# Optimization experiments

Measured on AMD Instinct MI355X. Metric: run time of the kernel, lower is better.

Reference implementation:

```python
import math
import jax, jax.numpy as jnp
import numpy as np

B, N, D, H, L = 8, 1024, 512, 8, 6
HD = D // H
FREQ = 256
K_LORENTZ = 1.0


def lorentz_projx(x, k=K_LORENTZ):
    # geoopt Lorentz.projx: x0 = sqrt(k + ||x_space||^2)
    space = x[..., 1:]
    x0 = jnp.sqrt(k + jnp.sum(space * space, axis=-1, keepdims=True))
    return jnp.concatenate([x0, space], axis=-1)


def layernorm(x, eps=1e-6):
    m = jnp.mean(x, axis=-1, keepdims=True)
    v = jnp.mean((x - m) ** 2, axis=-1, keepdims=True)
    return (x - m) / jnp.sqrt(v + eps)


def make_pe(n, d):
    pos = np.arange(n, dtype=np.float32)[:, None]
    div = np.exp(np.arange(0, d, 2, dtype=np.float32) * (-math.log(10000.0) / d))
    pe = np.zeros((n, d), dtype=np.float32)
    pe[:, 0::2] = np.sin(pos * div)
    pe[:, 1::2] = np.cos(pos * div)
    return jnp.asarray(pe)


def setup_inputs() -> dict:
    key = jax.random.key(0)
    ks = jax.random.split(key, 20)
    s = 0.02
    inp = {
        "t": jax.random.uniform(ks[0], (B,), jnp.float32) * 1000.0,
        "x": jax.random.normal(ks[1], (B, N, D), jnp.float32),
        "mask": jnp.ones((B, N), jnp.float32),
        "pe": make_pe(N, D),
        # timestep embedder MLP (weights stored [in,out])
        "tw1": jax.random.normal(ks[2], (FREQ, D), jnp.float32) * s,
        "tb1": jnp.zeros((D,), jnp.float32),
        "tw2": jax.random.normal(ks[3], (D, D), jnp.float32) * s,
        "tb2": jnp.zeros((D,), jnp.float32),
        # per-layer params stacked over L
        "Wq": jax.random.normal(ks[4], (L, D, D), jnp.float32) * s,
        "bq": jnp.zeros((L, D), jnp.float32),
        "Wk": jax.random.normal(ks[5], (L, D, D), jnp.float32) * s,
        "bk": jnp.zeros((L, D), jnp.float32),
        "Wv": jax.random.normal(ks[6], (L, D, D), jnp.float32) * s,
        "bv": jnp.zeros((L, D), jnp.float32),
        "W1": jax.random.normal(ks[7], (L, D, 4 * D), jnp.float32) * s,
        "b1": jnp.zeros((L, 4 * D), jnp.float32),
        "W2": jax.random.normal(ks[8], (L, 4 * D, D), jnp.float32) * s,
        "b2": jnp.zeros((L, D), jnp.float32),
        "Wada": jax.random.normal(ks[9], (L, D, 6 * D), jnp.float32) * s,
        "bada": jnp.zeros((L, 6 * D), jnp.float32),
    }
    return inp


def timestep_embedding(t, dim=FREQ, max_period=10000.0):
    half = dim // 2
    freqs = jnp.exp(-math.log(max_period) * jnp.arange(half, dtype=jnp.float32) / half)
    args = t[:, None] * freqs[None]
    return jnp.concatenate([jnp.cos(args), jnp.sin(args)], axis=-1)  # [B, dim]


def attention(h, mask, Wq, bq, Wk, bk, Wv, bv):
    # h: [B,N,D], mask: [B,N]
    q = (h @ Wq + bq).reshape(B, N, H, HD).transpose(0, 2, 1, 3)
    k = (h @ Wk + bk).reshape(B, N, H, HD).transpose(0, 2, 1, 3)
    v = (h @ Wv + bv).reshape(B, N, H, HD).transpose(0, 2, 1, 3)
    scores = jnp.einsum("bhqd,bhkd->bhqk", q, k) / math.sqrt(HD)
    # faithful quirk: valid positions get +1 added, invalid get -10000
    mm = jnp.einsum("bi,bj->bij", mask, mask)[:, None]  # [B,1,N,N]
    mm = jnp.where(mm == 0, -10000.0, mm)
    scores = scores + mm
    probs = jax.nn.softmax(scores, axis=-1)
    ctx = jnp.einsum("bhqk,bhkd->bhqd", probs, v)
    return ctx.transpose(0, 2, 1, 3).reshape(B, N, D)


def reference(t, x, mask, pe, tw1, tb1, tw2, tb2, Wq, bq, Wk, bk, Wv, bv,
              W1, b1, W2, b2, Wada, bada):
    # z = x + PositionalEncoding(x) = 2*x + pe
    z = x + (x + pe[None])
    # timestep embedder
    c = timestep_embedding(t) @ tw1 + tb1
    c = jax.nn.silu(c) @ tw2 + tb2  # [B, D]
    for i in range(L):
        ada = jax.nn.silu(c) @ Wada[i] + bada[i]  # [B, 6D]
        sh_msa, sc_msa, g_msa, sh_mlp, sc_mlp, g_mlp = jnp.split(ada, 6, axis=-1)
        h = layernorm(z) * (1.0 + sc_msa[:, None]) + sh_msa[:, None]
        z = z + g_msa[:, None] * attention(h, mask, Wq[i], bq[i], Wk[i], bk[i], Wv[i], bv[i])
        z = lorentz_projx(z)
        h = layernorm(z) * (1.0 + sc_mlp[:, None]) + sh_mlp[:, None]
        m = jax.nn.gelu(h @ W1[i] + b1[i], approximate=True) @ W2[i] + b2[i]
        z = z + g_mlp[:, None] * m
        z = lorentz_projx(z)
    z = lorentz_projx(z)
    return jnp.where(mask[:, :, None] != 0, z, 0.0)
```

## Files before the change

kernel.cpp:

```cpp
#include <hip/hip_runtime.h>
#include <hip/hip_bf16.h>
#include <math.h>

#define NTOK 1024
#define DMODEL 512
#define NHEAD 8
#define HDIM 64
#define BATCH 8
#define NLAYER 6
#define ROWS (BATCH*NTOK)
#define QKVSTR 1536
#define LOG2E 1.44269504f

typedef __attribute__((ext_vector_type(8))) short bf16x8;
typedef __attribute__((ext_vector_type(4))) float f32x4;
typedef unsigned short ushort_t;


__device__ __forceinline__ float silu_f(float x) { return x / (1.f + expf(-x)); }

__device__ __forceinline__ float gelu_tanh_f(float x) {
    float x3 = x * x * x;
    float y2 = 1.5957691216057308f * (x + 0.044715f * x3);
    float e = __builtin_amdgcn_exp2f(-y2 * LOG2E);
    return x / (1.f + e);
}

__device__ __forceinline__ unsigned short f2bf(float x) {
    __hip_bfloat16 b = __float2bfloat16(x);
    return *reinterpret_cast<unsigned short*>(&b);
}

__device__ __forceinline__ float bf2f(unsigned short u) {
    union { float f; unsigned v; } c;
    c.v = (unsigned)u << 16;
    return c.f;
}

template<int NW>
__device__ __forceinline__ float blk_sum(float v, volatile float* scratch) {
    #pragma unroll
    for (int o = 32; o > 0; o >>= 1) v += __shfl_down(v, o);
    if ((threadIdx.x & 63) == 0) scratch[threadIdx.x >> 6] = v;
    __syncthreads();
    float s = scratch[0];
    #pragma unroll
    for (int i = 1; i < NW; i++) s += scratch[i];
    __syncthreads();
    return s;
}


__global__ __launch_bounds__(256) void init_z_kernel(const float* __restrict__ x,
                                                     const float* __restrict__ pe,
                                                     float* __restrict__ z) {
    int i = blockIdx.x * 256 + threadIdx.x;
    const int C4 = DMODEL / 4;
    int row = i / C4;
    int col4 = i - row * C4;
    int n = row & (NTOK - 1);
    float4 xv = ((const float4*)x)[i];
    float4 pv = ((const float4*)pe)[n * C4 + col4];
    float4 o;
    o.x = 2.f * xv.x + pv.x;
    o.y = 2.f * xv.y + pv.y;
    o.z = 2.f * xv.z + pv.z;
    o.w = 2.f * xv.w + pv.w;
    ((float4*)z)[i] = o;
}

__global__ void temb_kernel(const float* __restrict__ t, float* __restrict__ temb) {
    int b = blockIdx.x;
    int j = threadIdx.x;
    float f = expf(-9.210340371976184f * (float)j / 128.f);
    float a = t[b] * f;
    temb[b * 256 + j] = cosf(a);
    temb[b * 256 + 128 + j] = sinf(a);
}

__global__ __launch_bounds__(256) void skinny_part(const float* __restrict__ A,
                                                   const float* __restrict__ W,
                                                   float* __restrict__ part,
                                                   int K, int N, int NL) {
    __shared__ float Als[8][128];
    const int l = blockIdx.z;
    const int n = blockIdx.x * 256 + threadIdx.x;
    const int kc = blockIdx.y;
    const int kbase = kc * 128;
    for (int i = threadIdx.x; i < 8 * 128; i += 256) {
        int b = i >> 7, k = i & 127;
        Als[b][k] = A[b * K + kbase + k];
    }
    __syncthreads();
    float acc[8] = {};
    const float* wp = W + (size_t)l * K * N + (size_t)kbase * N + n;
    for (int k = 0; k < 128; k += 4) {
        float w0 = wp[0];
        float w1 = wp[N];
        float w2 = wp[2 * N];
        float w3 = wp[3 * N];
        wp += 4 * (size_t)N;
        #pragma unroll
        for (int b = 0; b < 8; b++)
            acc[b] += Als[b][k] * w0 + Als[b][k + 1] * w1 + Als[b][k + 2] * w2 + Als[b][k + 3] * w3;
    }
    #pragma unroll
    for (int b = 0; b < 8; b++)
        part[((size_t)kc * 8 + b) * NL + (size_t)l * N + n] = acc[b];
}

template<int ACT>
__global__ __launch_bounds__(256) void skinny_reduce(const float* __restrict__ part,
                                                     const float* __restrict__ bias,
                                                     float* __restrict__ out,
                                                     int KC, int N, int NL) {
    int i = blockIdx.x * 256 + threadIdx.x;
    if (i >= 8 * NL) return;
    int b = i / NL, n = i - b * NL;
    float s = bias[n];
    for (int kc = 0; kc < KC; kc++) s += part[((size_t)kc * 8 + b) * NL + n];
    if (ACT == 1) s = silu_f(s);
    int l = n / N, nl = n - l * N;
    out[((size_t)l * 8 + b) * N + nl] = s;
}


__global__ __launch_bounds__(256) void transp_cvt3(const float* __restrict__ Wq,
                                                   const float* __restrict__ Wk,
                                                   const float* __restrict__ Wv,
                                                   ushort_t* __restrict__ dst) {
    __shared__ float tile[32][33];
    const float* src = blockIdx.z == 0 ? Wq : (blockIdx.z == 1 ? Wk : Wv);
    int k0 = blockIdx.y * 32, n0 = blockIdx.x * 32;
    int c = threadIdx.x & 31, r8 = threadIdx.x >> 5;
    #pragma unroll
    for (int i = 0; i < 4; i++) {
        int r = r8 + i * 8;
        tile[r][c] = src[(size_t)(k0 + r) * 512 + n0 + c];
    }
    __syncthreads();
    ushort_t* d = dst + (size_t)blockIdx.z * 512 * 512;
    #pragma unroll
    for (int i = 0; i < 4; i++) {
        int rr = r8 + i * 8;
        d[(size_t)(n0 + rr) * 512 + k0 + c] = f2bf(tile[c][rr]);
    }
}

__global__ __launch_bounds__(256) void transp_cvt(const float* __restrict__ src,
                                                  ushort_t* __restrict__ dst,
                                                  int K, int N) {
    __shared__ float tile[32][33];
    int k0 = blockIdx.y * 32, n0 = blockIdx.x * 32;
    int c = threadIdx.x & 31, r8 = threadIdx.x >> 5;
    #pragma unroll
    for (int i = 0; i < 4; i++) {
        int r = r8 + i * 8;
        tile[r][c] = src[(size_t)(k0 + r) * N + n0 + c];
    }
    __syncthreads();
    #pragma unroll
    for (int i = 0; i < 4; i++) {
        int rr = r8 + i * 8;
        dst[(size_t)(n0 + rr) * K + k0 + c] = f2bf(tile[c][rr]);
    }
}

__global__ void pack_bias(const float* __restrict__ bq, const float* __restrict__ bk,
                          const float* __restrict__ bv, float* __restrict__ bqkv) {
    int idx = blockIdx.x * 256 + threadIdx.x;
    if (idx >= NLAYER * QKVSTR) return;
    int l = idx / QKVSTR, n = idx - l * QKVSTR;
    float v = (n < 512) ? bq[l * 512 + n] : (n < 1024) ? bk[l * 512 + n - 512] : bv[l * 512 + n - 1024];
    bqkv[idx] = v;
}

template<int ACT, int OUTBF, int QPRESCALE>
__global__ __launch_bounds__(256) void mfma_gemm(const ushort_t* __restrict__ A,
                                                 const ushort_t* __restrict__ Bt,
                                                 const float* __restrict__ bias,
                                                 void* __restrict__ Cout,
                                                 int M, int N, int K) {
    __shared__ ushort_t Als[2][128 * 64];
    __shared__ ushort_t Bls[2][128 * 64];
    const int tid = threadIdx.x;
    const int lane = tid & 63, wv = tid >> 6;
    const int wm = (wv >> 1) * 64, wn = (wv & 1) * 64;
    const int lrow = lane & 15, lk = lane >> 4;
    const int m0 = blockIdx.x * 128, n0 = blockIdx.y * 128;
    const int srow = lane >> 3;
    const int qp = lane & 7;
    const int ql = qp ^ srow;

    f32x4 acc[4][4];
    #pragma unroll
    for (int i = 0; i < 4; i++)
        #pragma unroll
        for (int j = 0; j < 4; j++) {
            f32x4 zz = {0.f, 0.f, 0.f, 0.f};
            acc[i][j] = zz;
        }

    const int nK = K >> 6;

    auto STAGE = [&](int p, int ks) {
        const int k0 = ks << 6;
        #pragma unroll
        for (int it = 0; it < 4; it++) {
            int chunk = wv * 4 + it;
            int row = chunk * 8 + srow;
            const ushort_t* srcA = A + (size_t)(m0 + row) * K + k0 + ql * 8;
            const ushort_t* srcB = Bt + (size_t)(n0 + row) * K + k0 + ql * 8;
            __builtin_amdgcn_global_load_lds((const __attribute__((address_space(1))) void*)srcA,
                                             (__attribute__((address_space(3))) void*)(&Als[p][chunk * 512]),
                                             16, 0, 0);
            __builtin_amdgcn_global_load_lds((const __attribute__((address_space(1))) void*)srcB,
                                             (__attribute__((address_space(3))) void*)(&Bls[p][chunk * 512]),
                                             16, 0, 0);
        }
    };

    STAGE(0, 0);
    int cur = 0;
    for (int ks = 0; ks < nK; ks++) {
        if (ks + 1 < nK) {
            STAGE(cur ^ 1, ks + 1);
            asm volatile("s_waitcnt vmcnt(8)" ::: "memory");
        } else {
            asm volatile("s_waitcnt vmcnt(0)" ::: "memory");
        }
        __builtin_amdgcn_s_barrier();
        asm volatile("" ::: "memory");

        const ushort_t* Ab = &Als[cur][0];
        const ushort_t* Bb = &Bls[cur][0];
        #pragma unroll
        for (int kk = 0; kk < 2; kk++) {
            bf16x8 af[4], bfr[4];
            #pragma unroll
            for (int f = 0; f < 4; f++) {
                int ar = wm + f * 16 + lrow;
                af[f] = *(const bf16x8*)(Ab + ar * 64 + (((kk * 4 + lk) ^ (ar & 7)) << 3));
                int br = wn + f * 16 + lrow;
                bfr[f] = *(const bf16x8*)(Bb + br * 64 + (((kk * 4 + lk) ^ (br & 7)) << 3));
            }
            #pragma unroll
            for (int i = 0; i < 4; i++)
                #pragma unroll
                for (int j = 0; j < 4; j++)
                    acc[i][j] = __builtin_amdgcn_mfma_f32_16x16x32_bf16(af[i], bfr[j], acc[i][j], 0, 0, 0);
        }
        asm volatile("" ::: "memory");
        __builtin_amdgcn_s_barrier();
        cur ^= 1;
    }

    #pragma unroll
    for (int j = 0; j < 4; j++) {
        int col = n0 + wn + j * 16 + lrow;
        float bcol = bias[col];
        #pragma unroll
        for (int i = 0; i < 4; i++) {
            #pragma unroll
            for (int r = 0; r < 4; r++) {
                int row = m0 + wm + i * 16 + lk * 4 + r;
                float v = acc[i][j][r] + bcol;
                if (ACT == 1) v = gelu_tanh_f(v);
                if (QPRESCALE && col < 512) v *= 0.125f * LOG2E;
                if (OUTBF) ((ushort_t*)Cout)[(size_t)row * N + col] = f2bf(v);
                else       ((float*)Cout)[(size_t)row * N + col] = v;
            }
        }
    }
}


__global__ __launch_bounds__(128) void ln_mod_kernel(const float* __restrict__ z,
                                                     const float* __restrict__ ada,
                                                     ushort_t* __restrict__ out,
                                                     int sh_off, int sc_off) {
    __shared__ float red[2];
    int row = blockIdx.x;
    int b = row >> 10;
    int tid = threadIdx.x;
    float4 v = ((const float4*)(z + (size_t)row * DMODEL))[tid];
    float s = v.x + v.y + v.z + v.w;
    float mean = blk_sum<2>(s, red) * (1.f / DMODEL);
    float dx = v.x - mean, dy = v.y - mean, dz = v.z - mean, dw = v.w - mean;
    float ssq = dx * dx + dy * dy + dz * dz + dw * dw;
    float var = blk_sum<2>(ssq, red) * (1.f / DMODEL);
    float rstd = rsqrtf(var + 1e-6f);
    const float* ab = ada + b * (6 * DMODEL);
    float4 sc4 = ((const float4*)(ab + sc_off))[tid];
    float4 sh4 = ((const float4*)(ab + sh_off))[tid];
    unsigned short u0 = f2bf(dx * rstd * (1.f + sc4.x) + sh4.x);
    unsigned short u1 = f2bf(dy * rstd * (1.f + sc4.y) + sh4.y);
    unsigned short u2 = f2bf(dz * rstd * (1.f + sc4.z) + sh4.z);
    unsigned short u3 = f2bf(dw * rstd * (1.f + sc4.w) + sh4.w);
    uint2 pk;
    pk.x = (unsigned)u0 | ((unsigned)u1 << 16);
    pk.y = (unsigned)u2 | ((unsigned)u3 << 16);
    ((uint2*)(out + (size_t)row * DMODEL))[tid] = pk;
}

__global__ __launch_bounds__(128) void resid_ln_kernel(float* __restrict__ z,
                                                       const ushort_t* __restrict__ add,
                                                       const float* __restrict__ adaG, int g_off,
                                                       const float* __restrict__ adaLN, int sh_off, int sc_off,
                                                       ushort_t* __restrict__ out) {
    __shared__ float red[2];
    int row = blockIdx.x;
    int b = row >> 10;
    int tid = threadIdx.x;
    float4 v = ((float4*)(z + (size_t)row * DMODEL))[tid];
    uint2 a2 = ((const uint2*)(add + (size_t)row * DMODEL))[tid];
    float4 g4 = ((const float4*)(adaG + b * (6 * DMODEL) + g_off))[tid];
    v.x += g4.x * bf2f((unsigned short)(a2.x & 0xffff));
    v.y += g4.y * bf2f((unsigned short)(a2.x >> 16));
    v.z += g4.z * bf2f((unsigned short)(a2.y & 0xffff));
    v.w += g4.w * bf2f((unsigned short)(a2.y >> 16));
    float ssq = v.x * v.x + v.y * v.y + v.z * v.z + v.w * v.w;
    if (tid == 0) ssq -= v.x * v.x;
    float tot = blk_sum<2>(ssq, red);
    if (tid == 0) v.x = sqrtf(1.f + tot);
    ((float4*)(z + (size_t)row * DMODEL))[tid] = v;
    float s = v.x + v.y + v.z + v.w;
    float mean = blk_sum<2>(s, red) * (1.f / DMODEL);
    float dx = v.x - mean, dy = v.y - mean, dz = v.z - mean, dw = v.w - mean;
    float sq2 = dx * dx + dy * dy + dz * dz + dw * dw;
    float var = blk_sum<2>(sq2, red) * (1.f / DMODEL);
    float rstd = rsqrtf(var + 1e-6f);
    const float* ab = adaLN + b * (6 * DMODEL);
    float4 sc4 = ((const float4*)(ab + sc_off))[tid];
    float4 sh4 = ((const float4*)(ab + sh_off))[tid];
    unsigned short u0 = f2bf(dx * rstd * (1.f + sc4.x) + sh4.x);
    unsigned short u1 = f2bf(dy * rstd * (1.f + sc4.y) + sh4.y);
    unsigned short u2 = f2bf(dz * rstd * (1.f + sc4.z) + sh4.z);
    unsigned short u3 = f2bf(dw * rstd * (1.f + sc4.w) + sh4.w);
    uint2 pk;
    pk.x = (unsigned)u0 | ((unsigned)u1 << 16);
    pk.y = (unsigned)u2 | ((unsigned)u3 << 16);
    ((uint2*)(out + (size_t)row * DMODEL))[tid] = pk;
}

__global__ __launch_bounds__(128) void resid_final_kernel(const float* __restrict__ z,
                                                          const ushort_t* __restrict__ add,
                                                          const float* __restrict__ adaG, int g_off,
                                                          const float* __restrict__ mask,
                                                          float* __restrict__ out) {
    __shared__ float red[2];
    int row = blockIdx.x;
    int b = row >> 10;
    int tid = threadIdx.x;
    float4 v = ((const float4*)(z + (size_t)row * DMODEL))[tid];
    uint2 a2 = ((const uint2*)(add + (size_t)row * DMODEL))[tid];
    float4 g4 = ((const float4*)(adaG + b * (6 * DMODEL) + g_off))[tid];
    v.x += g4.x * bf2f((unsigned short)(a2.x & 0xffff));
    v.y += g4.y * bf2f((unsigned short)(a2.x >> 16));
    v.z += g4.z * bf2f((unsigned short)(a2.y & 0xffff));
    v.w += g4.w * bf2f((unsigned short)(a2.y >> 16));
    float ssq = v.x * v.x + v.y * v.y + v.z * v.z + v.w * v.w;
    if (tid == 0) ssq -= v.x * v.x;
    float tot = blk_sum<2>(ssq, red);
    if (tid == 0) v.x = sqrtf(1.f + tot);
    float m = mask[row];
    if (m == 0.f) { v.x = 0.f; v.y = 0.f; v.z = 0.f; v.w = 0.f; }
    ((float4*)(out + (size_t)row * DMODEL))[tid] = v;
}

__global__ __launch_bounds__(512) void flash_attn_mfma(const ushort_t* __restrict__ qkv,
                                                       const float* __restrict__ mask,
                                                       ushort_t* __restrict__ ctx) {
    __shared__ ushort_t Kls[64 * 64];
    __shared__ ushort_t Vt[64 * 64];
    __shared__ ushort_t Pls[8][16 * 64];
    __shared__ float Ms[64];

    const int tid = threadIdx.x;
    const int lane = tid & 63, w = tid >> 6;
    const int c = lane & 15, g = lane >> 4;
    const int bh = blockIdx.x;
    const int q0 = blockIdx.y * 128;
    const int b = bh >> 3, h = bh & 7;

    const ushort_t* qptr = qkv + (size_t)(b * NTOK + q0 + w * 16 + c) * QKVSTR + h * HDIM + g * 8;
    bf16x8 aq0 = *(const bf16x8*)(qptr);
    bf16x8 aq1 = *(const bf16x8*)(qptr + 32);

    const float mq = mask[b * NTOK + q0 + w * 16 + c];

    f32x4 o[4];
    #pragma unroll
    for (int j = 0; j < 4; j++) { f32x4 zz = {0.f,0.f,0.f,0.f}; o[j] = zz; }
    float m_run = -1e30f, l_run = 0.f;

    const int srow = lane >> 3, qp = lane & 7, ql = qp ^ srow;
    const int kp = tid & 31, dg = tid >> 5;

    char* Pw = (char*)&Pls[w][0];
    const int cswz = (c & 7) << 4;

    for (int kt = 0; kt < NTOK / 64; kt++) {
        const int k0 = kt * 64;
        __syncthreads();
        {
            int row = w * 8 + srow;
            const ushort_t* src = qkv + (size_t)(b * NTOK + k0 + row) * QKVSTR + 512 + h * HDIM + ql * 8;
            __builtin_amdgcn_global_load_lds((const __attribute__((address_space(1))) void*)src,
                                             (__attribute__((address_space(3))) void*)(Kls + w * 512),
                                             16, 0, 0);
        }
        {
            const ushort_t* v0 = qkv + (size_t)(b * NTOK + k0 + 2 * kp) * QKVSTR + 1024 + h * HDIM + dg * 4;
            uint2 r0 = *(const uint2*)v0;
            uint2 r1 = *(const uint2*)(v0 + QKVSTR);
            const ushort_t* e0 = (const ushort_t*)&r0;
            const ushort_t* e1 = (const ushort_t*)&r1;
            unsigned* VtU = (unsigned*)Vt;
            #pragma unroll
            for (int i = 0; i < 4; i++) {
                int d = dg * 4 + i;
                unsigned pk = (unsigned)e0[i] | ((unsigned)e1[i] << 16);
                VtU[d * 32 + (((kp >> 2) ^ (d & 7)) << 2) + (kp & 3)] = pk;
            }
        }
        if (tid < 64) Ms[tid] = mask[b * NTOK + k0 + tid];
        __syncthreads();

        f32x4 s[4];
        #pragma unroll
        for (int j = 0; j < 4; j++) { f32x4 zz = {0.f,0.f,0.f,0.f}; s[j] = zz; }
        __builtin_amdgcn_s_setprio(1);
        #pragma unroll
        for (int j = 0; j < 4; j++) {
            int row = j * 16 + c;
            bf16x8 ak0 = *(const bf16x8*)(Kls + row * 64 + ((g ^ (row & 7)) << 3));
            bf16x8 ak1 = *(const bf16x8*)(Kls + row * 64 + (((4 + g) ^ (row & 7)) << 3));
            s[j] = __builtin_amdgcn_mfma_f32_16x16x32_bf16(ak0, aq0, s[j], 0, 0, 0);
            s[j] = __builtin_amdgcn_mfma_f32_16x16x32_bf16(ak1, aq1, s[j], 0, 0, 0);
        }
        __builtin_amdgcn_s_setprio(0);

        float rm = -1e30f;
        #pragma unroll
        for (int j = 0; j < 4; j++) {
            float4 mk4 = *(const float4*)&Ms[j * 16 + 4 * g];
            const float* mkp = (const float*)&mk4;
            #pragma unroll
            for (int r = 0; r < 4; r++) {
                float mm = mq * mkp[r];
                s[j][r] += (mm == 0.f ? -14427.0f : mm * LOG2E);
                rm = fmaxf(rm, s[j][r]);
            }
        }
        rm = fmaxf(rm, __shfl_xor(rm, 16));
        rm = fmaxf(rm, __shfl_xor(rm, 32));

        if (!__all(rm - m_run <= 8.f)) {
            float mnew = fmaxf(m_run, rm);
            float scl = exp2f(m_run - mnew);
            m_run = mnew;
            float sclr[4];
            #pragma unroll
            for (int r = 0; r < 4; r++) sclr[r] = __shfl(scl, (g << 4) + 4 * g + r);
            #pragma unroll
            for (int j = 0; j < 4; j++)
                #pragma unroll
                for (int r = 0; r < 4; r++)
                    o[j][r] *= sclr[r];
            l_run *= scl;
        }

        float p[4][4];
        float rsum = 0.f;
        #pragma unroll
        for (int j = 0; j < 4; j++)
            #pragma unroll
            for (int r = 0; r < 4; r++) {
                p[j][r] = exp2f(s[j][r] - m_run);
                rsum += p[j][r];
            }
        rsum += __shfl_xor(rsum, 16);
        rsum += __shfl_xor(rsum, 32);
        l_run += rsum;

        #pragma unroll
        for (int j = 0; j < 4; j++) {
            uint2 pk2;
            pk2.x = (unsigned)f2bf(p[j][0]) | ((unsigned)f2bf(p[j][1]) << 16);
            pk2.y = (unsigned)f2bf(p[j][2]) | ((unsigned)f2bf(p[j][3]) << 16);
            *(uint2*)(Pw + c * 128 + ((j * 32 + g * 8) ^ cswz)) = pk2;
        }

        __builtin_amdgcn_s_setprio(1);
        #pragma unroll
        for (int kk = 0; kk < 2; kk++) {
            bf16x8 pa = *(const bf16x8*)(Pw + c * 128 + ((kk * 64 + g * 16) ^ cswz));
            #pragma unroll
            for (int j = 0; j < 4; j++) {
                int vr = j * 16 + c;
                bf16x8 bv = *(const bf16x8*)(Vt + vr * 64 + (((kk * 4 + g) ^ (vr & 7)) << 3));
                o[j] = __builtin_amdgcn_mfma_f32_16x16x32_bf16(pa, bv, o[j], 0, 0, 0);
            }
        }
        __builtin_amdgcn_s_setprio(0);
    }

    float invr[4];
    #pragma unroll
    for (int r = 0; r < 4; r++) invr[r] = 1.f / __shfl(l_run, (g << 4) + 4 * g + r);
    #pragma unroll
    for (int r = 0; r < 4; r++) {
        size_t row = (size_t)(b * NTOK + q0 + w * 16 + 4 * g + r) * DMODEL + h * HDIM;
        #pragma unroll
        for (int j = 0; j < 4; j++)
            ctx[row + j * 16 + c] = f2bf(o[j][r] * invr[r]);
    }
}


extern "C" void kernel_launch(void* const* d_in, const int* in_sizes, int n_in,
                              void* d_out, int out_size, void* d_ws, size_t ws_size,
                              hipStream_t stream) {
    const float* t    = (const float*)d_in[0];
    const float* x    = (const float*)d_in[1];
    const float* mask = (const float*)d_in[2];
    const float* pe   = (const float*)d_in[3];
    const float* tw1  = (const float*)d_in[4];
    const float* tb1  = (const float*)d_in[5];
    const float* tw2  = (const float*)d_in[6];
    const float* tb2  = (const float*)d_in[7];
    const float* Wq   = (const float*)d_in[8];
    const float* bq   = (const float*)d_in[9];
    const float* Wk   = (const float*)d_in[10];
    const float* bk   = (const float*)d_in[11];
    const float* Wv   = (const float*)d_in[12];
    const float* bv   = (const float*)d_in[13];
    const float* W1   = (const float*)d_in[14];
    const float* b1   = (const float*)d_in[15];
    const float* W2   = (const float*)d_in[16];
    const float* b2   = (const float*)d_in[17];
    const float* Wada = (const float*)d_in[18];
    const float* bada = (const float*)d_in[19];
    float* out = (float*)d_out;

    float* z      = (float*)d_ws;
    ushort_t* cxb = (ushort_t*)(z + (size_t)ROWS * DMODEL);
    ushort_t* qkv = cxb + (size_t)ROWS * DMODEL;
    ushort_t* mid = qkv;
    ushort_t* hb  = qkv + (size_t)ROWS * 2048;
    ushort_t* wqkv_t = hb + (size_t)ROWS * DMODEL;
    ushort_t* w1_t   = wqkv_t + 1536 * 512;
    ushort_t* w2_t   = w1_t + 2048 * 512;
    float* bqkv  = (float*)(w2_t + 512 * 2048);
    float* temb  = bqkv + NLAYER * QKVSTR;
    float* cmid  = temb + BATCH * 256;
    float* scs   = cmid + BATCH * DMODEL;
    float* part  = scs + BATCH * DMODEL;
    float* ada_all = part + 4 * 8 * (NLAYER * 3072);

    init_z_kernel<<<ROWS * DMODEL / 4 / 256, 256, 0, stream>>>(x, pe, z);
    temb_kernel<<<BATCH, 128, 0, stream>>>(t, temb);
    pack_bias<<<(NLAYER * QKVSTR + 255) / 256, 256, 0, stream>>>(bq, bk, bv, bqkv);

    skinny_part<<<dim3(2, 2, 1), 256, 0, stream>>>(temb, tw1, part, 256, 512, 512);
    skinny_reduce<1><<<16, 256, 0, stream>>>(part, tb1, cmid, 2, 512, 512);
    skinny_part<<<dim3(2, 4, 1), 256, 0, stream>>>(cmid, tw2, part, 512, 512, 512);
    skinny_reduce<1><<<16, 256, 0, stream>>>(part, tb2, scs, 4, 512, 512);
    skinny_part<<<dim3(12, 4, NLAYER), 256, 0, stream>>>(scs, Wada, part, 512, 3072, NLAYER * 3072);
    skinny_reduce<0><<<(8 * NLAYER * 3072 + 255) / 256, 256, 0, stream>>>(
        part, bada, ada_all, 4, 3072, NLAYER * 3072);

    dim3 gqkv(ROWS / 128, QKVSTR / 128);
    dim3 gmlp1(ROWS / 128, 2048 / 128);
    dim3 gmlp2(ROWS / 128, DMODEL / 128);
    dim3 ga(BATCH * NHEAD, NTOK / 128);

    ln_mod_kernel<<<ROWS, 128, 0, stream>>>(z, ada_all, hb, 0, 512);

    for (int i = 0; i < NLAYER; i++) {
        const float* ada = ada_all + (size_t)i * 8 * 3072;

        transp_cvt3<<<dim3(16, 16, 3), 256, 0, stream>>>(Wq + (size_t)i * 512 * 512,
                                                         Wk + (size_t)i * 512 * 512,
                                                         Wv + (size_t)i * 512 * 512, wqkv_t);
        transp_cvt<<<dim3(64, 16), 256, 0, stream>>>(W1 + (size_t)i * 512 * 2048, w1_t, 512, 2048);
        transp_cvt<<<dim3(16, 64), 256, 0, stream>>>(W2 + (size_t)i * 2048 * 512, w2_t, 2048, 512);

        mfma_gemm<0, 1, 1><<<gqkv, 256, 0, stream>>>(hb, wqkv_t, bqkv + i * QKVSTR, qkv,
                                                     ROWS, QKVSTR, DMODEL);

        flash_attn_mfma<<<ga, 512, 0, stream>>>(qkv, mask, cxb);

        resid_ln_kernel<<<ROWS, 128, 0, stream>>>(z, cxb, ada, 2 * DMODEL,
                                                  ada, 3 * DMODEL, 4 * DMODEL, hb);

        mfma_gemm<1, 1, 0><<<gmlp1, 256, 0, stream>>>(hb, w1_t, b1 + (size_t)i * 4 * DMODEL, mid,
                                                      ROWS, 4 * DMODEL, DMODEL);
        mfma_gemm<0, 1, 0><<<gmlp2, 256, 0, stream>>>(mid, w2_t, b2 + (size_t)i * DMODEL, cxb,
                                                      ROWS, DMODEL, 4 * DMODEL);

        if (i < NLAYER - 1) {
            const float* adan = ada_all + (size_t)(i + 1) * 8 * 3072;
            resid_ln_kernel<<<ROWS, 128, 0, stream>>>(z, cxb, ada, 5 * DMODEL,
                                                      adan, 0, 512, hb);
        } else {
            resid_final_kernel<<<ROWS, 128, 0, stream>>>(z, cxb, ada, 5 * DMODEL, mask, out);
        }
    }
}
```

Before: 1.062 ms.

## Merge weight transposes, stage GEMM epilogue via LDS, widen attention key tiles

Three weight transpose-convert launches per layer become one kernel that picks its matrix from the block index, which cuts launch overhead. The bf16 GEMM epilogue now writes the output tile into the reused shared buffer and then stores it with coalesced 16-byte writes, replacing scattered 2-byte stores. Flash attention processes 128 keys per iteration instead of 64, halving the number of loop barriers and using wider V loads, at the cost of more LDS and more registers for the score fragments.

Result: no change. 1.061 ms (-0.0%).

```diff
diff --git a/kernel.cpp b/kernel.cpp
--- a/kernel.cpp
+++ b/kernel.cpp
@@ -124,34 +124,32 @@
     out[((size_t)l * 8 + b) * N + nl] = s;
 }
 
-
-__global__ __launch_bounds__(256) void transp_cvt3(const float* __restrict__ Wq,
-                                                   const float* __restrict__ Wk,
-                                                   const float* __restrict__ Wv,
-                                                   ushort_t* __restrict__ dst) {
+__global__ __launch_bounds__(256) void transp_all(const float* __restrict__ Wq,
+                                                  const float* __restrict__ Wk,
+                                                  const float* __restrict__ Wv,
+                                                  const float* __restrict__ W1,
+                                                  const float* __restrict__ W2,
+                                                  ushort_t* __restrict__ wqkv_t,
+                                                  ushort_t* __restrict__ w1_t,
+                                                  ushort_t* __restrict__ w2_t) {
     __shared__ float tile[32][33];
-    const float* src = blockIdx.z == 0 ? Wq : (blockIdx.z == 1 ? Wk : Wv);
-    int k0 = blockIdx.y * 32, n0 = blockIdx.x * 32;
-    int c = threadIdx.x & 31, r8 = threadIdx.x >> 5;
-    #pragma unroll
-    for (int i = 0; i < 4; i++) {
-        int r = r8 + i * 8;
-        tile[r][c] = src[(size_t)(k0 + r) * 512 + n0 + c];
-    }
-    __syncthreads();
-    ushort_t* d = dst + (size_t)blockIdx.z * 512 * 512;
-    #pragma unroll
-    for (int i = 0; i < 4; i++) {
-        int rr = r8 + i * 8;
-        d[(size_t)(n0 + rr) * 512 + k0 + c] = f2bf(tile[c][rr]);
-    }
-}
-
-__global__ __launch_bounds__(256) void transp_cvt(const float* __restrict__ src,
-                                                  ushort_t* __restrict__ dst,
-                                                  int K, int N) {
-    __shared__ float tile[32][33];
-    int k0 = blockIdx.y * 32, n0 = blockIdx.x * 32;
+    int blk = blockIdx.x;
+    const float* src; ushort_t* dst; int K, N, k0, n0;
+    if (blk < 768) {
+        int zz = blk >> 8, rem = blk & 255;
+        k0 = (rem >> 4) * 32; n0 = (rem & 15) * 32;
+        src = zz == 0 ? Wq : (zz == 1 ? Wk : Wv);
+        dst = wqkv_t + zz * 512 * 512;
+        K = 512; N = 512;
+    } else if (blk < 1792) {
+        int rem = blk - 768;
+        n0 = (rem & 63) * 32; k0 = (rem >> 6) * 32;
+        src = W1; dst = w1_t; K = 512; N = 2048;
+    } else {
+        int rem = blk - 1792;
+        n0 = (rem & 15) * 32; k0 = (rem >> 4) * 32;
+        src = W2; dst = w2_t; K = 2048; N = 512;
+    }
     int c = threadIdx.x & 31, r8 = threadIdx.x >> 5;
     #pragma unroll
     for (int i = 0; i < 4; i++) {
@@ -181,8 +179,7 @@
                                                  const float* __restrict__ bias,
                                                  void* __restrict__ Cout,
                                                  int M, int N, int K) {
-    __shared__ ushort_t Als[2][128 * 64];
-    __shared__ ushort_t Bls[2][128 * 64];
+    __shared__ ushort_t smem[4 * 128 * 64];
     const int tid = threadIdx.x;
     const int lane = tid & 63, wv = tid >> 6;
     const int wm = (wv >> 1) * 64, wn = (wv & 1) * 64;
@@ -205,6 +202,8 @@
 
     auto STAGE = [&](int p, int ks) {
         const int k0 = ks << 6;
+        ushort_t* Ad = smem + p * 8192;
+        ushort_t* Bd = smem + 16384 + p * 8192;
         #pragma unroll
         for (int it = 0; it < 4; it++) {
             int chunk = wv * 4 + it;
@@ -212,10 +211,10 @@
             const ushort_t* srcA = A + (size_t)(m0 + row) * K + k0 + ql * 8;
             const ushort_t* srcB = Bt + (size_t)(n0 + row) * K + k0 + ql * 8;
             __builtin_amdgcn_global_load_lds((const __attribute__((address_space(1))) void*)srcA,
-                                             (__attribute__((address_space(3))) void*)(&Als[p][chunk * 512]),
+                                             (__attribute__((address_space(3))) void*)(Ad + chunk * 512),
                                              16, 0, 0);
             __builtin_amdgcn_global_load_lds((const __attribute__((address_space(1))) void*)srcB,
-                                             (__attribute__((address_space(3))) void*)(&Bls[p][chunk * 512]),
+                                             (__attribute__((address_space(3))) void*)(Bd + chunk * 512),
                                              16, 0, 0);
         }
     };
@@ -232,8 +231,8 @@
         __builtin_amdgcn_s_barrier();
         asm volatile("" ::: "memory");
 
-        const ushort_t* Ab = &Als[cur][0];
-        const ushort_t* Bb = &Bls[cur][0];
+        const ushort_t* Ab = smem + cur * 8192;
+        const ushort_t* Bb = smem + 16384 + cur * 8192;
         #pragma unroll
         for (int kk = 0; kk < 2; kk++) {
             bf16x8 af[4], bfr[4];
@@ -255,21 +254,47 @@
         cur ^= 1;
     }
 
-    #pragma unroll
-    for (int j = 0; j < 4; j++) {
-        int col = n0 + wn + j * 16 + lrow;
-        float bcol = bias[col];
-        #pragma unroll
-        for (int i = 0; i < 4; i++) {
-            #pragma unroll
-            for (int r = 0; r < 4; r++) {
-                int row = m0 + wm + i * 16 + lk * 4 + r;
-                float v = acc[i][j][r] + bcol;
-                if (ACT == 1) v = gelu_tanh_f(v);
-                if (QPRESCALE && col < 512) v *= 0.125f * LOG2E;
-                if (OUTBF) ((ushort_t*)Cout)[(size_t)row * N + col] = f2bf(v);
-                else       ((float*)Cout)[(size_t)row * N + col] = v;
+    if (OUTBF) {
+        __syncthreads();
+        #pragma unroll
+        for (int j = 0; j < 4; j++) {
+            int coll = wn + j * 16 + lrow;
+            float bcol = bias[n0 + coll];
+            #pragma unroll
+            for (int i = 0; i < 4; i++) {
+                #pragma unroll
+                for (int r = 0; r < 4; r++) {
+                    int rowl = wm + i * 16 + lk * 4 + r;
+                    float v = acc[i][j][r] + bcol;
+                    if (ACT == 1) v = gelu_tanh_f(v);
+                    if (QPRESCALE && (n0 + coll) < 512) v *= 0.125f * LOG2E;
+                    smem[rowl * 136 + coll] = f2bf(v);
+                }
             }
+        }
+        __syncthreads();
+        ushort_t* Co = (ushort_t*)Cout;
+        #pragma unroll
+        for (int pass = 0; pass < 8; pass++) {
+            int rowl = pass * 16 + (tid >> 4);
+            int cseg = (tid & 15) * 8;
+            uint4 vv = *(const uint4*)(smem + rowl * 136 + cseg);
+            *(uint4*)(Co + (size_t)(m0 + rowl) * N + n0 + cseg) = vv;
+        }
+    } else {
+        #pragma unroll
+        for (int j = 0; j < 4; j++) {
+            int col = n0 + wn + j * 16 + lrow;
+            float bcol = bias[col];
+            #pragma unroll
+            for (int i = 0; i < 4; i++)
+                #pragma unroll
+                for (int r = 0; r < 4; r++) {
+                    int row = m0 + wm + i * 16 + lk * 4 + r;
+                    float v = acc[i][j][r] + bcol;
+                    if (ACT == 1) v = gelu_tanh_f(v);
+                    ((float*)Cout)[(size_t)row * N + col] = v;
+                }
         }
     }
 }
@@ -371,10 +396,10 @@
 __global__ __launch_bounds__(512) void flash_attn_mfma(const ushort_t* __restrict__ qkv,
                                                        const float* __restrict__ mask,
                                                        ushort_t* __restrict__ ctx) {
-    __shared__ ushort_t Kls[64 * 64];
-    __shared__ ushort_t Vt[64 * 64];
-    __shared__ ushort_t Pls[8][16 * 64];
-    __shared__ float Ms[64];
+    __shared__ ushort_t Kls[128 * 64];
+    __shared__ ushort_t Vt[64 * 128];
+    __shared__ ushort_t Pls[8][16 * 128];
+    __shared__ float Ms[128];
 
     const int tid = threadIdx.x;
     const int lane = tid & 63, w = tid >> 6;
@@ -395,44 +420,46 @@
     float m_run = -1e30f, l_run = 0.f;
 
     const int srow = lane >> 3, qp = lane & 7, ql = qp ^ srow;
-    const int kp = tid & 31, dg = tid >> 5;
+    const int kp = tid & 63, dg = tid >> 6;
 
     char* Pw = (char*)&Pls[w][0];
     const int cswz = (c & 7) << 4;
 
-    for (int kt = 0; kt < NTOK / 64; kt++) {
-        const int k0 = kt * 64;
+    for (int kt = 0; kt < NTOK / 128; kt++) {
+        const int k0 = kt * 128;
         __syncthreads();
-        {
-            int row = w * 8 + srow;
+        #pragma unroll
+        for (int it = 0; it < 2; it++) {
+            int chunk = w * 2 + it;
+            int row = chunk * 8 + srow;
             const ushort_t* src = qkv + (size_t)(b * NTOK + k0 + row) * QKVSTR + 512 + h * HDIM + ql * 8;
             __builtin_amdgcn_global_load_lds((const __attribute__((address_space(1))) void*)src,
-                                             (__attribute__((address_space(3))) void*)(Kls + w * 512),
+                                             (__attribute__((address_space(3))) void*)(Kls + chunk * 512),
                                              16, 0, 0);
         }
         {
-            const ushort_t* v0 = qkv + (size_t)(b * NTOK + k0 + 2 * kp) * QKVSTR + 1024 + h * HDIM + dg * 4;
-            uint2 r0 = *(const uint2*)v0;
-            uint2 r1 = *(const uint2*)(v0 + QKVSTR);
+            const ushort_t* v0 = qkv + (size_t)(b * NTOK + k0 + 2 * kp) * QKVSTR + 1024 + h * HDIM + dg * 8;
+            uint4 r0 = *(const uint4*)v0;
+            uint4 r1 = *(const uint4*)(v0 + QKVSTR);
             const ushort_t* e0 = (const ushort_t*)&r0;
             const ushort_t* e1 = (const ushort_t*)&r1;
             unsigned* VtU = (unsigned*)Vt;
             #pragma unroll
-            for (int i = 0; i < 4; i++) {
-                int d = dg * 4 + i;
+            for (int i = 0; i < 8; i++) {
+                int d = dg * 8 + i;
                 unsigned pk = (unsigned)e0[i] | ((unsigned)e1[i] << 16);
-                VtU[d * 32 + (((kp >> 2) ^ (d & 7)) << 2) + (kp & 3)] = pk;
+                VtU[d * 64 + (((kp >> 2) ^ (d & 7)) << 2) + (kp & 3)] = pk;
             }
         }
-        if (tid < 64) Ms[tid] = mask[b * NTOK + k0 + tid];
+        if (tid < 128) Ms[tid] = mask[b * NTOK + k0 + tid];
         __syncthreads();
 
-        f32x4 s[4];
-        #pragma unroll
-        for (int j = 0; j < 4; j++) { f32x4 zz = {0.f,0.f,0.f,0.f}; s[j] = zz; }
+        f32x4 s[8];
+        #pragma unroll
+        for (int j = 0; j < 8; j++) { f32x4 zz = {0.f,0.f,0.f,0.f}; s[j] = zz; }
         __builtin_amdgcn_s_setprio(1);
         #pragma unroll
-        for (int j = 0; j < 4; j++) {
+        for (int j = 0; j < 8; j++) {
             int row = j * 16 + c;
             bf16x8 ak0 = *(const bf16x8*)(Kls + row * 64 + ((g ^ (row & 7)) << 3));
             bf16x8 ak1 = *(const bf16x8*)(Kls + row * 64 + (((4 + g) ^ (row & 7)) << 3));
@@ -443,7 +470,7 @@
 
         float rm = -1e30f;
         #pragma unroll
-        for (int j = 0; j < 4; j++) {
+        for (int j = 0; j < 8; j++) {
             float4 mk4 = *(const float4*)&Ms[j * 16 + 4 * g];
             const float* mkp = (const float*)&mk4;
             #pragma unroll
@@ -471,35 +498,31 @@
             l_run *= scl;
         }
 
-        float p[4][4];
         float rsum = 0.f;
         #pragma unroll
-        for (int j = 0; j < 4; j++)
-            #pragma unroll
-            for (int r = 0; r < 4; r++) {
-                p[j][r] = exp2f(s[j][r] - m_run);
-                rsum += p[j][r];
-            }
+        for (int j = 0; j < 8; j++) {
+            float p0 = exp2f(s[j][0] - m_run);
+            float p1 = exp2f(s[j][1] - m_run);
+            float p2 = exp2f(s[j][2] - m_run);
+            float p3 = exp2f(s[j][3] - m_run);
+            rsum += (p0 + p1) + (p2 + p3);
+            uint2 pk2;
+            pk2.x = (unsigned)f2bf(p0) | ((unsigned)f2bf(p1) << 16);
+            pk2.y = (unsigned)f2bf(p2) | ((unsigned)f2bf(p3) << 16);
+            *(uint2*)(Pw + c * 256 + ((j * 32 + g * 8) ^ cswz)) = pk2;
+        }
         rsum += __shfl_xor(rsum, 16);
         rsum += __shfl_xor(rsum, 32);
         l_run += rsum;
 
-        #pragma unroll
-        for (int j = 0; j < 4; j++) {
-            uint2 pk2;
-            pk2.x = (unsigned)f2bf(p[j][0]) | ((unsigned)f2bf(p[j][1]) << 16);
-            pk2.y = (unsigned)f2bf(p[j][2]) | ((unsigned)f2bf(p[j][3]) << 16);
-            *(uint2*)(Pw + c * 128 + ((j * 32 + g * 8) ^ cswz)) = pk2;
-        }
-
         __builtin_amdgcn_s_setprio(1);
         #pragma unroll
-        for (int kk = 0; kk < 2; kk++) {
-            bf16x8 pa = *(const bf16x8*)(Pw + c * 128 + ((kk * 64 + g * 16) ^ cswz));
+        for (int kk = 0; kk < 4; kk++) {
+            bf16x8 pa = *(const bf16x8*)(Pw + c * 256 + ((kk * 64 + g * 16) ^ cswz));
             #pragma unroll
             for (int j = 0; j < 4; j++) {
                 int vr = j * 16 + c;
-                bf16x8 bv = *(const bf16x8*)(Vt + vr * 64 + (((kk * 4 + g) ^ (vr & 7)) << 3));
+                bf16x8 bv = *(const bf16x8*)(Vt + vr * 128 + (((kk * 4 + g) ^ (vr & 7)) << 3));
                 o[j] = __builtin_amdgcn_mfma_f32_16x16x32_bf16(pa, bv, o[j], 0, 0, 0);
             }
         }
@@ -581,11 +604,12 @@
     for (int i = 0; i < NLAYER; i++) {
         const float* ada = ada_all + (size_t)i * 8 * 3072;
 
-        transp_cvt3<<<dim3(16, 16, 3), 256, 0, stream>>>(Wq + (size_t)i * 512 * 512,
-                                                         Wk + (size_t)i * 512 * 512,
-                                                         Wv + (size_t)i * 512 * 512, wqkv_t);
-        transp_cvt<<<dim3(64, 16), 256, 0, stream>>>(W1 + (size_t)i * 512 * 2048, w1_t, 512, 2048);
-        transp_cvt<<<dim3(16, 64), 256, 0, stream>>>(W2 + (size_t)i * 2048 * 512, w2_t, 2048, 512);
+        transp_all<<<2816, 256, 0, stream>>>(Wq + (size_t)i * 512 * 512,
+                                             Wk + (size_t)i * 512 * 512,
+                                             Wv + (size_t)i * 512 * 512,
+                                             W1 + (size_t)i * 512 * 2048,
+                                             W2 + (size_t)i * 2048 * 512,
+                                             wqkv_t, w1_t, w2_t);
 
         mfma_gemm<0, 1, 1><<<gqkv, 256, 0, stream>>>(hb, wqkv_t, bqkv + i * QKVSTR, qkv,
                                                      ROWS, QKVSTR, DMODEL);
```
